# Performance work log

Hardware: AMD Instinct MI355X
Metric: run time of the kernel (lower is better)

Reference implementation:

```python
import jax, jax.numpy as jnp
import numpy as np

B, C, H, W = 16, 256, 64, 64
DA = 64  # attention_size


def setup_inputs() -> dict:
    key = jax.random.key(0)
    ks = jax.random.split(key, 7)
    s_in = 1.0 / np.sqrt(C)
    return {
        "x": jax.random.normal(ks[0], (B, C, H, W), jnp.float32),
        "Wq": jax.random.normal(ks[1], (DA, C), jnp.float32) * s_in,
        "bq": jax.random.normal(ks[2], (DA,), jnp.float32) * 0.01,
        "Wk": jax.random.normal(ks[3], (DA, C), jnp.float32) * s_in,
        "bk": jax.random.normal(ks[4], (DA,), jnp.float32) * 0.01,
        "Wv": jax.random.normal(ks[5], (C, C), jnp.float32) * s_in,
        "bv": jax.random.normal(ks[6], (C,), jnp.float32) * 0.01,
    }


def reference(x, Wq, bq, Wk, bk, Wv, bv):
    b, c, h, w = x.shape
    n = h * w
    xf = x.reshape(b, c, n)                      # [B,C,N]
    q = jnp.einsum('ac,bcn->ban', Wq, xf) + bq[None, :, None]   # [B,DA,N]
    k = jnp.einsum('ac,bcn->ban', Wk, xf) + bk[None, :, None]   # [B,DA,N]
    v = jnp.einsum('dc,bcn->bdn', Wv, xf) + bv[None, :, None]   # [B,C,N]
    # scores[b,i,j] = q[:,i] . k[:,j], scaled by 1/sqrt(H*W) (as in source)
    scores = jnp.einsum('bai,baj->bij', q, k) / jnp.sqrt(jnp.float32(n))
    attn = jax.nn.softmax(scores, axis=-1)       # [B,N,N]
    out = jnp.einsum('bcj,bij->bci', v, attn)    # [B,C,N]
    return out.reshape(b, c, h, w) + x
```

## Files before the change

kernel.cpp:

```cpp
#include <hip/hip_runtime.h>
#include <hip/hip_bf16.h>
#include <stdint.h>


#define B_  16
#define C_  256
#define N_  4096
#define DA_ 64
#define MSHIFT 2.0f

typedef __attribute__((ext_vector_type(8))) short short8;
typedef __attribute__((ext_vector_type(4))) float f32x4;

__device__ int g_isf32;

__device__ __forceinline__ short f2bf(float f) {
    union { float f; uint32_t u; } v; v.f = f;
    uint32_t r = v.u + 0x7fffu + ((v.u >> 16) & 1u);
    return (short)(r >> 16);
}
__device__ __forceinline__ float bf2f(uint16_t s) {
    union { uint32_t u; float f; } v; v.u = ((uint32_t)s) << 16;
    return v.f;
}
__device__ __forceinline__ uint32_t pkbf(float a, float b) {
    union { __hip_bfloat162 h; uint32_t u; } c;
    c.h = __float22bfloat162_rn(make_float2(a, b));
    return c.u;
}

__global__ void detect_kernel(const void* __restrict__ x) {
    const uint16_t* p = (const uint16_t*)x;
    int i = threadIdx.x;
    uint16_t u = p[2 * i];
    int e = (u >> 7) & 0xFF;
    unsigned long long m = __ballot(e >= 112 && e <= 132);
    if (i == 0) g_isf32 = (__popcll(m) < 32) ? 1 : 0;
}

template<bool F32>
__device__ __forceinline__ void proj_body(
    const void* __restrict__ xv,
    const void* __restrict__ Wqv, const void* __restrict__ bqv,
    const void* __restrict__ Wkv, const void* __restrict__ bkv,
    const void* __restrict__ Wvv, const void* __restrict__ bvv,
    uint16_t* __restrict__ Q, uint16_t* __restrict__ K, uint16_t* __restrict__ Vt,
    float* bias_lds, uint16_t* buf)
{
    const int tid = threadIdx.x;
    const int b  = blockIdx.x >> 6;
    const int n0 = (blockIdx.x & 63) * 64;
    const int w = tid >> 6, lane = tid & 63, q = lane >> 4, ln = lane & 15;

    for (int idx = tid; idx < 384; idx += 256) {
        float bias;
        if (F32) {
            bias = (idx < 64)  ? ((const float*)bqv)[idx]
                 : (idx < 128) ? ((const float*)bkv)[idx - 64]
                               : ((const float*)bvv)[idx - 128];
        } else {
            bias = (idx < 64)  ? bf2f(((const uint16_t*)bqv)[idx])
                 : (idx < 128) ? bf2f(((const uint16_t*)bkv)[idx - 64])
                               : bf2f(((const uint16_t*)bvv)[idx - 128]);
        }
        bias_lds[idx] = bias;
    }

    {
        int cbase = tid >> 2, s0 = tid & 3;
        #pragma unroll
        for (int cc = 0; cc < 4; cc++) {
            int c = cc * 64 + cbase;
            if (F32) {
                const float* xr = (const float*)xv + ((size_t)b * C_ + c) * N_ + n0;
                #pragma unroll
                for (int k = 0; k < 4; k++) {
                    int nl = (s0 + 4 * k) * 4;
                    float4 v = *(const float4*)(xr + nl);
                    buf[(nl + 0) * 264 + c] = (uint16_t)f2bf(v.x);
                    buf[(nl + 1) * 264 + c] = (uint16_t)f2bf(v.y);
                    buf[(nl + 2) * 264 + c] = (uint16_t)f2bf(v.z);
                    buf[(nl + 3) * 264 + c] = (uint16_t)f2bf(v.w);
                }
            } else {
                const uint16_t* xr = (const uint16_t*)xv + ((size_t)b * C_ + c) * N_ + n0;
                #pragma unroll
                for (int k = 0; k < 2; k++) {
                    int nl = s0 * 16 + k * 8;
                    short8 v = *(const short8*)(xr + nl);
                    #pragma unroll
                    for (int e = 0; e < 8; e++)
                        buf[(nl + e) * 264 + c] = (uint16_t)v[e];
                }
            }
        }
    }
    __syncthreads();

    f32x4 acc[6][4];
    #pragma unroll
    for (int mt = 0; mt < 6; mt++)
        #pragma unroll
        for (int nt = 0; nt < 4; nt++) acc[mt][nt] = (f32x4)0.0f;

    for (int kc = 0; kc < 8; kc++) {
        short8 af[6];
        #pragma unroll
        for (int mt = 0; mt < 6; mt++) {
            int row = (w * 6 + mt) * 16 + ln;
            if (F32) {
                const float* src = (row < 64) ? (const float*)Wqv + (size_t)row * 256
                                 : (row < 128) ? (const float*)Wkv + (size_t)(row - 64) * 256
                                               : (const float*)Wvv + (size_t)(row - 128) * 256;
                float4 a0 = *(const float4*)(src + kc * 32 + q * 8);
                float4 a1 = *(const float4*)(src + kc * 32 + q * 8 + 4);
                union { short8 s; uint32_t u[4]; } c;
                c.u[0] = pkbf(a0.x, a0.y); c.u[1] = pkbf(a0.z, a0.w);
                c.u[2] = pkbf(a1.x, a1.y); c.u[3] = pkbf(a1.z, a1.w);
                af[mt] = c.s;
            } else {
                const uint16_t* src = (row < 64) ? (const uint16_t*)Wqv + (size_t)row * 256
                                    : (row < 128) ? (const uint16_t*)Wkv + (size_t)(row - 64) * 256
                                                  : (const uint16_t*)Wvv + (size_t)(row - 128) * 256;
                af[mt] = *(const short8*)(src + kc * 32 + q * 8);
            }
        }
        short8 bfr[4];
        #pragma unroll
        for (int nt = 0; nt < 4; nt++)
            bfr[nt] = *(const short8*)&buf[(nt * 16 + ln) * 264 + kc * 32 + q * 8];
        #pragma unroll
        for (int mt = 0; mt < 6; mt++)
            #pragma unroll
            for (int nt = 0; nt < 4; nt++)
                acc[mt][nt] = __builtin_amdgcn_mfma_f32_16x16x32_bf16(
                    af[mt], bfr[nt], acc[mt][nt], 0, 0, 0);
    }
    __syncthreads();

    #pragma unroll
    for (int mt = 0; mt < 6; mt++) {
        int rowb = (w * 6 + mt) * 16 + q * 4;
        #pragma unroll
        for (int r = 0; r < 4; r++) {
            float bias = bias_lds[rowb + r];
            #pragma unroll
            for (int nt = 0; nt < 4; nt++)
                buf[(rowb + r) * 72 + nt * 16 + ln] =
                    (uint16_t)f2bf(acc[mt][nt][r] + bias);
        }
    }
    __syncthreads();

    {
        int a = tid & 63, nb = tid >> 6;
        uint16_t* Qb = Q + ((size_t)b * N_ + n0) * 64;
        uint16_t* Kb = K + ((size_t)b * N_ + n0) * 64;
        #pragma unroll 4
        for (int j = 0; j < 16; j++) {
            int n = nb + 4 * j;
            Qb[(size_t)n * 64 + a] = buf[a * 72 + n];
            Kb[(size_t)n * 64 + a] = buf[(64 + a) * 72 + n];
        }
    }
    {
        int ch = tid & 7;
        #pragma unroll
        for (int p = 0; p < 8; p++) {
            int c = p * 32 + (tid >> 3);
            short8 v = *(const short8*)&buf[(128 + c) * 72 + ch * 8];
            *(short8*)(Vt + ((size_t)b * C_ + c) * N_ + n0 + ch * 8) = v;
        }
    }
}

__global__ __launch_bounds__(256, 2) void proj_kernel(
    const void* xv, const void* Wqv, const void* bqv, const void* Wkv,
    const void* bkv, const void* Wvv, const void* bvv,
    uint16_t* Q, uint16_t* K, uint16_t* Vt)
{
    __shared__ float    bias_lds[384];
    __shared__ uint16_t buf[384 * 72];
    if (g_isf32) proj_body<true >(xv, Wqv, bqv, Wkv, bkv, Wvv, bvv, Q, K, Vt, bias_lds, buf);
    else         proj_body<false>(xv, Wqv, bqv, Wkv, bkv, Wvv, bvv, Q, K, Vt, bias_lds, buf);
}

template<bool F32>
__device__ __forceinline__ void flash_body(
    const uint16_t* __restrict__ Q, const uint16_t* __restrict__ K,
    const uint16_t* __restrict__ Vt, const void* __restrict__ xv,
    void* __restrict__ outv,
    uint16_t* Klds2, uint16_t* Plds2, float* l_lds)
{
    const int tid = threadIdx.x;
    const int d  = blockIdx.x;
    const int xc = d & 7, rest = d >> 3;
    const int b  = xc + ((rest >= 64) ? 8 : 0);
    const int i0 = (rest & 63) * 64;
    const int w = tid >> 6, lane = tid & 63, q = lane >> 4, ln = lane & 15;

    const float c1 = 1.4426950408889634f / 64.0f;

    short8 qf[2];
    {
        const uint16_t* qrow = Q + ((size_t)b * N_ + (i0 + w * 16 + ln)) * 64;
        qf[0] = *(const short8*)(qrow + q * 8);
        qf[1] = *(const short8*)(qrow + 32 + q * 8);
    }

    const uint16_t* Kb = K + (size_t)b * N_ * 64;
    const uint16_t* vr0 = Vt + ((size_t)b * C_ + (w * 64 +  0 + ln)) * N_ + q * 8;
    const uint16_t* vr1 = Vt + ((size_t)b * C_ + (w * 64 + 16 + ln)) * N_ + q * 8;
    const uint16_t* vr2 = Vt + ((size_t)b * C_ + (w * 64 + 32 + ln)) * N_ + q * 8;
    const uint16_t* vr3 = Vt + ((size_t)b * C_ + (w * 64 + 48 + ln)) * N_ + q * 8;

    const int krow = tid >> 2, kc4 = tid & 3;
    const size_t kgoff = (size_t)krow * 64 + (size_t)(kc4 * 8);
    const int kg0 = ((krow >> 4) * 128 + kc4 * 16 + (krow & 15)) * 8;

    const int pbase = (w * 128 + (q >> 1) * 16 + ln) * 8 + (q & 1) * 4;

    float l_run = 0.0f;
    f32x4 O[4][4];
    #pragma unroll
    for (int rg = 0; rg < 4; rg++)
        #pragma unroll
        for (int ct = 0; ct < 4; ct++) O[rg][ct] = (f32x4)0.0f;

    {
        short8 k0 = *(const short8*)(Kb + kgoff);
        short8 k1 = *(const short8*)(Kb + kgoff + 32);
        *(short8*)&Klds2[kg0]       = k0;
        *(short8*)&Klds2[kg0 + 512] = k1;
    }
    __syncthreads();

    for (int it = 0; it < 64; it++) {
        const int j0 = it * 64;
        const int cur = it & 1;
        const uint16_t* Kc = Klds2 + cur * 4096;
        uint16_t*       Kn = Klds2 + (cur ^ 1) * 4096;
        uint16_t*       Pl = Plds2 + cur * 4096;

        short8 kreg0, kreg1;
        if (it < 63) {
            kreg0 = *(const short8*)(Kb + (size_t)(j0 + 64) * 64 + kgoff);
            kreg1 = *(const short8*)(Kb + (size_t)(j0 + 64) * 64 + kgoff + 32);
        }

        short8 v00 = *(const short8*)(vr0 + j0);
        short8 v01 = *(const short8*)(vr1 + j0);
        short8 v02 = *(const short8*)(vr2 + j0);
        short8 v03 = *(const short8*)(vr3 + j0);
        short8 v10 = *(const short8*)(vr0 + j0 + 32);
        short8 v11 = *(const short8*)(vr1 + j0 + 32);
        short8 v12 = *(const short8*)(vr2 + j0 + 32);
        short8 v13 = *(const short8*)(vr3 + j0 + 32);

        f32x4 s[4];
        #pragma unroll
        for (int jt = 0; jt < 4; jt++) s[jt] = (f32x4)0.0f;
        #pragma unroll
        for (int jt = 0; jt < 4; jt++) {
            short8 kf0 = *(const short8*)&Kc[lane * 8 + jt * 1024];
            s[jt] = __builtin_amdgcn_mfma_f32_16x16x32_bf16(kf0, qf[0], s[jt], 0, 0, 0);
            short8 kf1 = *(const short8*)&Kc[lane * 8 + jt * 1024 + 512];
            s[jt] = __builtin_amdgcn_mfma_f32_16x16x32_bf16(kf1, qf[1], s[jt], 0, 0, 0);
        }

        #pragma unroll
        for (int jt = 0; jt < 4; jt++) {
            float p0 = exp2f(s[jt][0] * c1 - MSHIFT);
            float p1 = exp2f(s[jt][1] * c1 - MSHIFT);
            float p2 = exp2f(s[jt][2] * c1 - MSHIFT);
            float p3 = exp2f(s[jt][3] * c1 - MSHIFT);
            l_run += (p0 + p1) + (p2 + p3);
            uint2 pk; pk.x = pkbf(p0, p1); pk.y = pkbf(p2, p3);
            *(uint2*)&Pl[pbase + jt * 256] = pk;
        }

        if (it < 63) {
            asm volatile("s_waitcnt vmcnt(0)" ::: "memory");
            *(short8*)&Kn[kg0]       = kreg0;
            *(short8*)&Kn[kg0 + 512] = kreg1;
        }

        asm volatile("s_waitcnt lgkmcnt(0)\n\ts_barrier" ::: "memory");

        {
            short8 af[4];
            #pragma unroll
            for (int rg = 0; rg < 4; rg++)
                af[rg] = *(const short8*)&Pl[lane * 8 + rg * 1024];
            #pragma unroll
            for (int rg = 0; rg < 4; rg++) {
                O[rg][0] = __builtin_amdgcn_mfma_f32_16x16x32_bf16(af[rg], v00, O[rg][0], 0, 0, 0);
                O[rg][1] = __builtin_amdgcn_mfma_f32_16x16x32_bf16(af[rg], v01, O[rg][1], 0, 0, 0);
                O[rg][2] = __builtin_amdgcn_mfma_f32_16x16x32_bf16(af[rg], v02, O[rg][2], 0, 0, 0);
                O[rg][3] = __builtin_amdgcn_mfma_f32_16x16x32_bf16(af[rg], v03, O[rg][3], 0, 0, 0);
            }
            #pragma unroll
            for (int rg = 0; rg < 4; rg++)
                af[rg] = *(const short8*)&Pl[lane * 8 + rg * 1024 + 512];
            #pragma unroll
            for (int rg = 0; rg < 4; rg++) {
                O[rg][0] = __builtin_amdgcn_mfma_f32_16x16x32_bf16(af[rg], v10, O[rg][0], 0, 0, 0);
                O[rg][1] = __builtin_amdgcn_mfma_f32_16x16x32_bf16(af[rg], v11, O[rg][1], 0, 0, 0);
                O[rg][2] = __builtin_amdgcn_mfma_f32_16x16x32_bf16(af[rg], v12, O[rg][2], 0, 0, 0);
                O[rg][3] = __builtin_amdgcn_mfma_f32_16x16x32_bf16(af[rg], v13, O[rg][3], 0, 0, 0);
            }
        }
    }

    l_run += __shfl_xor(l_run, 16);
    l_run += __shfl_xor(l_run, 32);
    if (lane < 16) l_lds[w * 16 + lane] = l_run;
    __syncthreads();

    #pragma unroll
    for (int rg = 0; rg < 4; rg++) {
        f32x4 lv = *(const f32x4*)&l_lds[rg * 16 + q * 4];
        f32x4 li; li[0] = 1.0f/lv[0]; li[1] = 1.0f/lv[1]; li[2] = 1.0f/lv[2]; li[3] = 1.0f/lv[3];
        #pragma unroll
        for (int ct = 0; ct < 4; ct++) {
            int c = w * 64 + ct * 16 + ln;
            size_t off = (size_t)c * N_ + i0 + rg * 16 + q * 4;
            if (F32) {
                const float* xb = (const float*)xv + (size_t)b * C_ * N_;
                float* ob = (float*)outv + (size_t)b * C_ * N_;
                float4 xv4 = *(const float4*)(xb + off);
                float4 res;
                res.x = O[rg][ct][0] * li[0] + xv4.x;
                res.y = O[rg][ct][1] * li[1] + xv4.y;
                res.z = O[rg][ct][2] * li[2] + xv4.z;
                res.w = O[rg][ct][3] * li[3] + xv4.w;
                *(float4*)(ob + off) = res;
            } else {
                const uint16_t* xb = (const uint16_t*)xv + (size_t)b * C_ * N_;
                uint16_t* ob = (uint16_t*)outv + (size_t)b * C_ * N_;
                uint2 xp = *(const uint2*)(xb + off);
                uint2 res;
                res.x = pkbf(O[rg][ct][0] * li[0] + bf2f((uint16_t)(xp.x & 0xFFFF)),
                             O[rg][ct][1] * li[1] + bf2f((uint16_t)(xp.x >> 16)));
                res.y = pkbf(O[rg][ct][2] * li[2] + bf2f((uint16_t)(xp.y & 0xFFFF)),
                             O[rg][ct][3] * li[3] + bf2f((uint16_t)(xp.y >> 16)));
                *(uint2*)(ob + off) = res;
            }
        }
    }
}

__global__ __launch_bounds__(256, 3) void flash_kernel(
    const uint16_t* Q, const uint16_t* K, const uint16_t* Vt,
    const void* xv, void* outv)
{
    __shared__ uint16_t Klds2[2 * 4096];
    __shared__ uint16_t Plds2[2 * 4096];
    __shared__ __align__(16) float l_lds[64];
    if (g_isf32) flash_body<true >(Q, K, Vt, xv, outv, Klds2, Plds2, l_lds);
    else         flash_body<false>(Q, K, Vt, xv, outv, Klds2, Plds2, l_lds);
}

extern "C" void kernel_launch(void* const* d_in, const int* in_sizes, int n_in,
                              void* d_out, int out_size, void* d_ws, size_t ws_size,
                              hipStream_t stream) {
    const void* x  = d_in[0];
    const void* Wq = d_in[1];
    const void* bq = d_in[2];
    const void* Wk = d_in[3];
    const void* bk = d_in[4];
    const void* Wv = d_in[5];
    const void* bv = d_in[6];

    uint16_t* Qw = (uint16_t*)d_ws;
    uint16_t* Kw = Qw + (size_t)B_ * N_ * DA_;
    uint16_t* Vw = Kw + (size_t)B_ * N_ * DA_;

    detect_kernel<<<dim3(1), dim3(64), 0, stream>>>(x);
    proj_kernel<<<dim3(B_ * 64), dim3(256), 0, stream>>>(x, Wq, bq, Wk, bk, Wv, bv, Qw, Kw, Vw);
    flash_kernel<<<dim3(B_ * 64), dim3(256), 0, stream>>>(Qw, Kw, Vw, x, d_out);
}
```

Baseline: 435.2 us.

## Software-pipeline attention loop so PV of tile overlaps QK of next tile

Restructures the main attention loop into a prologue, steady state and epilogue. Each iteration computes the score MFMAs for tile it+1 while running the P·V MFMAs for tile it, and V fragments are prefetched one tile ahead. The K prefetch now runs two tiles ahead with a partial vmcnt wait, and the K global-to-LDS copy mapping is changed so each wave loads the rows it writes. The aim is to hide global load latency and the exp/softmax VALU work behind MFMA, leaving one barrier per iteration. In exchange it raises register pressure from holding V fragments and scores across iterations, and correctness relies on the hand-counted vmcnt(8).

Measured after the change: 467.7 us. 7.5% more time.

```diff
diff --git a/kernel.cpp b/kernel.cpp
--- a/kernel.cpp
+++ b/kernel.cpp
@@ -214,9 +214,9 @@
     const uint16_t* vr2 = Vt + ((size_t)b * C_ + (w * 64 + 32 + ln)) * N_ + q * 8;
     const uint16_t* vr3 = Vt + ((size_t)b * C_ + (w * 64 + 48 + ln)) * N_ + q * 8;
 
-    const int krow = tid >> 2, kc4 = tid & 3;
-    const size_t kgoff = (size_t)krow * 64 + (size_t)(kc4 * 8);
-    const int kg0 = ((krow >> 4) * 128 + kc4 * 16 + (krow & 15)) * 8;
+    const int ln2 = tid & 15, kc4 = (tid >> 4) & 3;
+    const size_t kgoff = (size_t)(w * 16 + ln2) * 64 + (size_t)(kc4 * 8);
+    const int kg0 = (w * 128 + kc4 * 16 + ln2) * 8;
 
     const int pbase = (w * 128 + (q >> 1) * 16 + ln) * 8 + (q & 1) * 4;
 
@@ -235,37 +235,85 @@
     }
     __syncthreads();
 
-    for (int it = 0; it < 64; it++) {
+    short8 kreg0 = *(const short8*)(Kb + (size_t)64 * 64 + kgoff);
+    short8 kreg1 = *(const short8*)(Kb + (size_t)64 * 64 + kgoff + 32);
+    short8 v00 = *(const short8*)(vr0);
+    short8 v01 = *(const short8*)(vr1);
+    short8 v02 = *(const short8*)(vr2);
+    short8 v03 = *(const short8*)(vr3);
+    short8 v10 = *(const short8*)(vr0 + 32);
+    short8 v11 = *(const short8*)(vr1 + 32);
+    short8 v12 = *(const short8*)(vr2 + 32);
+    short8 v13 = *(const short8*)(vr3 + 32);
+
+    f32x4 s[4];
+
+    #pragma unroll
+    for (int jt = 0; jt < 4; jt++) {
+        s[jt] = (f32x4)0.0f;
+        short8 kf0 = *(const short8*)&Klds2[lane * 8 + jt * 1024];
+        s[jt] = __builtin_amdgcn_mfma_f32_16x16x32_bf16(kf0, qf[0], s[jt], 0, 0, 0);
+        short8 kf1 = *(const short8*)&Klds2[lane * 8 + jt * 1024 + 512];
+        s[jt] = __builtin_amdgcn_mfma_f32_16x16x32_bf16(kf1, qf[1], s[jt], 0, 0, 0);
+    }
+    #pragma unroll
+    for (int jt = 0; jt < 4; jt++) {
+        float p0 = exp2f(s[jt][0] * c1 - MSHIFT);
+        float p1 = exp2f(s[jt][1] * c1 - MSHIFT);
+        float p2 = exp2f(s[jt][2] * c1 - MSHIFT);
+        float p3 = exp2f(s[jt][3] * c1 - MSHIFT);
+        l_run += (p0 + p1) + (p2 + p3);
+        uint2 pk; pk.x = pkbf(p0, p1); pk.y = pkbf(p2, p3);
+        *(uint2*)&Plds2[pbase + jt * 256] = pk;
+    }
+    asm volatile("s_waitcnt vmcnt(8)" ::: "memory");
+    *(short8*)&Klds2[4096 + kg0]       = kreg0;
+    *(short8*)&Klds2[4096 + kg0 + 512] = kreg1;
+    asm volatile("s_waitcnt lgkmcnt(0)\n\ts_barrier" ::: "memory");
+
+    for (int it = 0; it < 63; ++it) {
         const int j0 = it * 64;
-        const int cur = it & 1;
-        const uint16_t* Kc = Klds2 + cur * 4096;
-        uint16_t*       Kn = Klds2 + (cur ^ 1) * 4096;
-        uint16_t*       Pl = Plds2 + cur * 4096;
-
-        short8 kreg0, kreg1;
-        if (it < 63) {
-            kreg0 = *(const short8*)(Kb + (size_t)(j0 + 64) * 64 + kgoff);
-            kreg1 = *(const short8*)(Kb + (size_t)(j0 + 64) * 64 + kgoff + 32);
-        }
-
-        short8 v00 = *(const short8*)(vr0 + j0);
-        short8 v01 = *(const short8*)(vr1 + j0);
-        short8 v02 = *(const short8*)(vr2 + j0);
-        short8 v03 = *(const short8*)(vr3 + j0);
-        short8 v10 = *(const short8*)(vr0 + j0 + 32);
-        short8 v11 = *(const short8*)(vr1 + j0 + 32);
-        short8 v12 = *(const short8*)(vr2 + j0 + 32);
-        short8 v13 = *(const short8*)(vr3 + j0 + 32);
-
-        f32x4 s[4];
-        #pragma unroll
-        for (int jt = 0; jt < 4; jt++) s[jt] = (f32x4)0.0f;
+        const uint16_t* Kcn = Klds2 + ((it + 1) & 1) * 4096;
+        uint16_t*       Kn  = Klds2 + (it & 1) * 4096;
+        const uint16_t* Plc = Plds2 + (it & 1) * 4096;
+        uint16_t*       Pln = Plds2 + ((it + 1) & 1) * 4096;
+
+        if (it < 62) {
+            kreg0 = *(const short8*)(Kb + (size_t)(j0 + 128) * 64 + kgoff);
+            kreg1 = *(const short8*)(Kb + (size_t)(j0 + 128) * 64 + kgoff + 32);
+        }
+
         #pragma unroll
         for (int jt = 0; jt < 4; jt++) {
-            short8 kf0 = *(const short8*)&Kc[lane * 8 + jt * 1024];
+            s[jt] = (f32x4)0.0f;
+            short8 kf0 = *(const short8*)&Kcn[lane * 8 + jt * 1024];
             s[jt] = __builtin_amdgcn_mfma_f32_16x16x32_bf16(kf0, qf[0], s[jt], 0, 0, 0);
-            short8 kf1 = *(const short8*)&Kc[lane * 8 + jt * 1024 + 512];
+            short8 kf1 = *(const short8*)&Kcn[lane * 8 + jt * 1024 + 512];
             s[jt] = __builtin_amdgcn_mfma_f32_16x16x32_bf16(kf1, qf[1], s[jt], 0, 0, 0);
+        }
+
+        {
+            short8 af[4];
+            #pragma unroll
+            for (int rg = 0; rg < 4; rg++)
+                af[rg] = *(const short8*)&Plc[lane * 8 + rg * 1024];
+            #pragma unroll
+            for (int rg = 0; rg < 4; rg++) {
+                O[rg][0] = __builtin_amdgcn_mfma_f32_16x16x32_bf16(af[rg], v00, O[rg][0], 0, 0, 0);
+                O[rg][1] = __builtin_amdgcn_mfma_f32_16x16x32_bf16(af[rg], v01, O[rg][1], 0, 0, 0);
+                O[rg][2] = __builtin_amdgcn_mfma_f32_16x16x32_bf16(af[rg], v02, O[rg][2], 0, 0, 0);
+                O[rg][3] = __builtin_amdgcn_mfma_f32_16x16x32_bf16(af[rg], v03, O[rg][3], 0, 0, 0);
+            }
+            #pragma unroll
+            for (int rg = 0; rg < 4; rg++)
+                af[rg] = *(const short8*)&Plc[lane * 8 + rg * 1024 + 512];
+            #pragma unroll
+            for (int rg = 0; rg < 4; rg++) {
+                O[rg][0] = __builtin_amdgcn_mfma_f32_16x16x32_bf16(af[rg], v10, O[rg][0], 0, 0, 0);
+                O[rg][1] = __builtin_amdgcn_mfma_f32_16x16x32_bf16(af[rg], v11, O[rg][1], 0, 0, 0);
+                O[rg][2] = __builtin_amdgcn_mfma_f32_16x16x32_bf16(af[rg], v12, O[rg][2], 0, 0, 0);
+                O[rg][3] = __builtin_amdgcn_mfma_f32_16x16x32_bf16(af[rg], v13, O[rg][3], 0, 0, 0);
+            }
         }
 
         #pragma unroll
@@ -276,39 +324,48 @@
             float p3 = exp2f(s[jt][3] * c1 - MSHIFT);
             l_run += (p0 + p1) + (p2 + p3);
             uint2 pk; pk.x = pkbf(p0, p1); pk.y = pkbf(p2, p3);
-            *(uint2*)&Pl[pbase + jt * 256] = pk;
-        }
-
-        if (it < 63) {
-            asm volatile("s_waitcnt vmcnt(0)" ::: "memory");
+            *(uint2*)&Pln[pbase + jt * 256] = pk;
+        }
+
+        v00 = *(const short8*)(vr0 + j0 + 64);
+        v01 = *(const short8*)(vr1 + j0 + 64);
+        v02 = *(const short8*)(vr2 + j0 + 64);
+        v03 = *(const short8*)(vr3 + j0 + 64);
+        v10 = *(const short8*)(vr0 + j0 + 96);
+        v11 = *(const short8*)(vr1 + j0 + 96);
+        v12 = *(const short8*)(vr2 + j0 + 96);
+        v13 = *(const short8*)(vr3 + j0 + 96);
+
+        if (it < 62) {
+            asm volatile("s_waitcnt vmcnt(8)" ::: "memory");
             *(short8*)&Kn[kg0]       = kreg0;
             *(short8*)&Kn[kg0 + 512] = kreg1;
         }
-
         asm volatile("s_waitcnt lgkmcnt(0)\n\ts_barrier" ::: "memory");
-
-        {
-            short8 af[4];
-            #pragma unroll
-            for (int rg = 0; rg < 4; rg++)
-                af[rg] = *(const short8*)&Pl[lane * 8 + rg * 1024];
-            #pragma unroll
-            for (int rg = 0; rg < 4; rg++) {
-                O[rg][0] = __builtin_amdgcn_mfma_f32_16x16x32_bf16(af[rg], v00, O[rg][0], 0, 0, 0);
-                O[rg][1] = __builtin_amdgcn_mfma_f32_16x16x32_bf16(af[rg], v01, O[rg][1], 0, 0, 0);
-                O[rg][2] = __builtin_amdgcn_mfma_f32_16x16x32_bf16(af[rg], v02, O[rg][2], 0, 0, 0);
-                O[rg][3] = __builtin_amdgcn_mfma_f32_16x16x32_bf16(af[rg], v03, O[rg][3], 0, 0, 0);
-            }
-            #pragma unroll
-            for (int rg = 0; rg < 4; rg++)
-                af[rg] = *(const short8*)&Pl[lane * 8 + rg * 1024 + 512];
-            #pragma unroll
-            for (int rg = 0; rg < 4; rg++) {
-                O[rg][0] = __builtin_amdgcn_mfma_f32_16x16x32_bf16(af[rg], v10, O[rg][0], 0, 0, 0);
-                O[rg][1] = __builtin_amdgcn_mfma_f32_16x16x32_bf16(af[rg], v11, O[rg][1], 0, 0, 0);
-                O[rg][2] = __builtin_amdgcn_mfma_f32_16x16x32_bf16(af[rg], v12, O[rg][2], 0, 0, 0);
-                O[rg][3] = __builtin_amdgcn_mfma_f32_16x16x32_bf16(af[rg], v13, O[rg][3], 0, 0, 0);
-            }
+    }
+
+    {
+        const uint16_t* Plc = Plds2 + 4096;
+        short8 af[4];
+        #pragma unroll
+        for (int rg = 0; rg < 4; rg++)
+            af[rg] = *(const short8*)&Plc[lane * 8 + rg * 1024];
+        #pragma unroll
+        for (int rg = 0; rg < 4; rg++) {
+            O[rg][0] = __builtin_amdgcn_mfma_f32_16x16x32_bf16(af[rg], v00, O[rg][0], 0, 0, 0);
+            O[rg][1] = __builtin_amdgcn_mfma_f32_16x16x32_bf16(af[rg], v01, O[rg][1], 0, 0, 0);
+            O[rg][2] = __builtin_amdgcn_mfma_f32_16x16x32_bf16(af[rg], v02, O[rg][2], 0, 0, 0);
+            O[rg][3] = __builtin_amdgcn_mfma_f32_16x16x32_bf16(af[rg], v03, O[rg][3], 0, 0, 0);
+        }
+        #pragma unroll
+        for (int rg = 0; rg < 4; rg++)
+            af[rg] = *(const short8*)&Plc[lane * 8 + rg * 1024 + 512];
+        #pragma unroll
+        for (int rg = 0; rg < 4; rg++) {
+            O[rg][0] = __builtin_amdgcn_mfma_f32_16x16x32_bf16(af[rg], v10, O[rg][0], 0, 0, 0);
+            O[rg][1] = __builtin_amdgcn_mfma_f32_16x16x32_bf16(af[rg], v11, O[rg][1], 0, 0, 0);
+            O[rg][2] = __builtin_amdgcn_mfma_f32_16x16x32_bf16(af[rg], v12, O[rg][2], 0, 0, 0);
+            O[rg][3] = __builtin_amdgcn_mfma_f32_16x16x32_bf16(af[rg], v13, O[rg][3], 0, 0, 0);
         }
     }
 
```
